# Performance work log

Hardware: AMD Instinct MI355X
Metric: run time of the kernel (lower is better)

The kernel has to match this reference:

```python
import jax, jax.numpy as jnp
import numpy as np

N, F_IN, HID, NH1, NCLS = 8192, 256, 64, 4, 16
LRELU_ALPHA = 0.2  # tf.nn.leaky_relu default


def setup_inputs() -> dict:
    key = jax.random.key(0)
    ks = jax.random.split(key, 12)
    s = 0.05
    seq = jax.random.normal(ks[0], (1, N, F_IN), jnp.float32)
    # sparse-ish adjacency -> additive mask bias (0 on edges, -1e9 elsewhere)
    adj = jax.random.uniform(ks[1], (N, N)) < 0.005
    adj = adj | jnp.eye(N, dtype=bool)
    bias_mat = jnp.where(adj, 0.0, -1e9).astype(jnp.float32)[None]  # [1,N,N]
    return {
        "seq": seq,
        "bias_mat": bias_mat,
        "W1": jax.random.normal(ks[2], (NH1, F_IN, HID), jnp.float32) * s,
        "a1_src": jax.random.normal(ks[3], (NH1, HID, 1), jnp.float32) * s,
        "a1_dst": jax.random.normal(ks[4], (NH1, HID, 1), jnp.float32) * s,
        "b1_src": jnp.zeros((NH1, 1), jnp.float32),
        "b1_dst": jnp.zeros((NH1, 1), jnp.float32),
        "bias1": jnp.zeros((NH1, HID), jnp.float32),
        "W2": jax.random.normal(ks[5], (1, NH1 * HID, NCLS), jnp.float32) * s,
        "a2_src": jax.random.normal(ks[6], (1, NCLS, 1), jnp.float32) * s,
        "a2_dst": jax.random.normal(ks[7], (1, NCLS, 1), jnp.float32) * s,
        "b2_src": jnp.zeros((1, 1), jnp.float32),
        "b2_dst": jnp.zeros((1, 1), jnp.float32),
        "bias2": jnp.zeros((1, NCLS), jnp.float32),
    }


def _gat_layer(x, bias_mat, W, a_src, a_dst, b_src, b_dst, bias_out):
    # x: [N, Fin]; W: [nh, Fin, H]; bias_mat: [1, N, N]
    fts = jnp.einsum('nf,hfd->hnd', x, W)                      # Conv1D(k=1, no bias)
    f1 = jnp.einsum('hnd,hdo->hno', fts, a_src) + b_src[:, None, :]  # [nh,N,1]
    f2 = jnp.einsum('hnd,hdo->hno', fts, a_dst) + b_dst[:, None, :]  # [nh,N,1]
    logits = f1 + jnp.swapaxes(f2, 1, 2)                       # [nh,N,N]
    coefs = jax.nn.softmax(jax.nn.leaky_relu(logits, LRELU_ALPHA) + bias_mat, axis=-1)
    vals = jnp.einsum('hnm,hmd->hnd', coefs, fts)              # [nh,N,H]
    return vals + bias_out[:, None, :]


def reference(seq, bias_mat, W1, a1_src, a1_dst, b1_src, b1_dst, bias1,
              W2, a2_src, a2_dst, b2_src, b2_dst, bias2):
    x = seq[0]  # [N, F_IN]; batch dim is 1
    # layer 1: NH1 heads, elu activation, concat over heads
    h = jax.nn.elu(_gat_layer(x, bias_mat, W1, a1_src, a1_dst, b1_src, b1_dst, bias1))
    h1 = jnp.transpose(h, (1, 0, 2)).reshape(N, NH1 * HID)     # tf.concat(heads, -1)
    # output layer: 1 head, identity activation, averaged over final heads (=1)
    out = _gat_layer(h1, bias_mat, W2, a2_src, a2_dst, b2_src, b2_dst, bias2)
    logits = out[0] / 1.0                                      # add_n/final_sum
    return logits[None]  # [1, N, NCLS]
```

## Files before the change

### kernel.cpp

```cpp
#include <hip/hip_runtime.h>
#include <hip/hip_bf16.h>
#include <math.h>

#define NN   8192
#define FIN  256
#define HID  64
#define NH   4
#define NC   16
#define MAXD 128
#define ALPHA 0.2f

__global__ __launch_bounds__(256) void k_scan_gemm(
    const float* __restrict__ bias, const float* __restrict__ seq,
    const float* __restrict__ W1, const float* __restrict__ a1s,
    const float* __restrict__ a1d, const float* __restrict__ b1s,
    const float* __restrict__ b1d,
    int* __restrict__ deg, int* __restrict__ cols,
    float* __restrict__ fts1, float* __restrict__ f1v, float* __restrict__ f2v)
{
    __shared__ float xs[64][68];
    __shared__ union {
        float w[64][68];
        struct { float r1[64][17]; float r2[64][17]; } red;
    } U;

    const int bid = blockIdx.x;
    const int t   = threadIdx.x;

    if (bid >= 512) {
        const int wv = t >> 6, lane = t & 63;
        const int row = (bid - 512) * 4 + wv;
        const float4* rp = (const float4*)(bias + (size_t)row * NN);
        int* crow = cols + (size_t)row * MAXD;
        const unsigned long long lt = (1ull << lane) - 1ull;
        int base = 0;
        for (int mit = 0; mit < 8; ++mit) {
            float4 vv[4];
            #pragma unroll
            for (int q = 0; q < 4; ++q) vv[q] = rp[mit*256 + q*64 + lane];
            #pragma unroll
            for (int q = 0; q < 4; ++q) {
                const float4 v = vv[q];
                const unsigned long long m0 = __ballot(v.x == 0.f);
                const unsigned long long m1 = __ballot(v.y == 0.f);
                const unsigned long long m2 = __ballot(v.z == 0.f);
                const unsigned long long m3 = __ballot(v.w == 0.f);
                int p = base + __popcll(m0&lt) + __popcll(m1&lt)
                             + __popcll(m2&lt) + __popcll(m3&lt);
                const int colbase = mit*1024 + q*256 + lane*4;
                if (v.x == 0.f) { if (p < MAXD) crow[p] = colbase;     ++p; }
                if (v.y == 0.f) { if (p < MAXD) crow[p] = colbase + 1; ++p; }
                if (v.z == 0.f) { if (p < MAXD) crow[p] = colbase + 2; ++p; }
                if (v.w == 0.f) { if (p < MAXD) crow[p] = colbase + 3; ++p; }
                base += __popcll(m0) + __popcll(m1) + __popcll(m2) + __popcll(m3);
            }
        }
        if (lane == 0) deg[row] = base < MAXD ? base : MAXD;
        return;
    }

    const int head    = bid & 3;
    const int rowbase = (bid >> 2) * 64;
    const int tr = t >> 4, tc = t & 15;

    float acc[4][4] = {};
    for (int kc = 0; kc < 4; ++kc) {
        #pragma unroll
        for (int i = 0; i < 4; ++i) {
            const int lin = t + i*256;
            const int r = lin >> 4, kq = lin & 15;
            const float4 v = *(const float4*)(seq + (size_t)(rowbase + r)*FIN + kc*64 + kq*4);
            *(float4*)&xs[r][kq*4] = v;
        }
        #pragma unroll
        for (int i = 0; i < 4; ++i) {
            const int lin = t + i*256;
            const int k = lin >> 4, dq = lin & 15;
            const float4 v = *(const float4*)(W1 + ((size_t)head*FIN + kc*64 + k)*HID + dq*4);
            *(float4*)&U.w[k][dq*4] = v;
        }
        __syncthreads();
        #pragma unroll 8
        for (int k = 0; k < 64; ++k) {
            const float4 bb = *(const float4*)&U.w[k][tc*4];
            #pragma unroll
            for (int i = 0; i < 4; ++i) {
                const float a = xs[tr*4 + i][k];
                acc[i][0] += a * bb.x; acc[i][1] += a * bb.y;
                acc[i][2] += a * bb.z; acc[i][3] += a * bb.w;
            }
        }
        __syncthreads();
    }

    float p1[4], p2[4];
    #pragma unroll
    for (int i = 0; i < 4; ++i) {
        const int node = rowbase + tr*4 + i;
        float4 o; o.x = acc[i][0]; o.y = acc[i][1]; o.z = acc[i][2]; o.w = acc[i][3];
        *(float4*)&fts1[((size_t)node*NH + head)*HID + tc*4] = o;
        float s1 = 0.f, s2 = 0.f;
        #pragma unroll
        for (int j = 0; j < 4; ++j) {
            s1 += acc[i][j] * a1s[head*HID + tc*4 + j];
            s2 += acc[i][j] * a1d[head*HID + tc*4 + j];
        }
        p1[i] = s1; p2[i] = s2;
    }
    #pragma unroll
    for (int i = 0; i < 4; ++i) {
        U.red.r1[tr*4 + i][tc] = p1[i];
        U.red.r2[tr*4 + i][tc] = p2[i];
    }
    __syncthreads();
    if (t < 64) {
        float s1 = b1s[head], s2 = b1d[head];
        #pragma unroll
        for (int q = 0; q < 16; ++q) { s1 += U.red.r1[t][q]; s2 += U.red.r2[t][q]; }
        const int node = rowbase + t;
        f1v[node*NH + head] = s1;
        f2v[node*NH + head] = s2;
    }
}

__global__ __launch_bounds__(256) void k_attn1(
    const float* __restrict__ fts1, const float* __restrict__ f1v,
    const float* __restrict__ f2v, const float* __restrict__ bias1,
    const float* __restrict__ W2, const float* __restrict__ a2s,
    const float* __restrict__ a2d, const float* __restrict__ b2s,
    const float* __restrict__ b2d,
    const int* __restrict__ deg, const int* __restrict__ cols,
    float* __restrict__ fts2, float* __restrict__ g1, float* __restrict__ g2)
{
    __shared__ int   colsS[MAXD];
    __shared__ float coefS[NH][MAXD];
    __shared__ float h1row[NH*HID];
    __shared__ float red[16][17];
    __shared__ float fts2S[NC];

    const int i = blockIdx.x;
    const int t = threadIdx.x, h = t >> 6, lane = t & 63;
    const int d = deg[i];
    for (int e = t; e < MAXD; e += 256) colsS[e] = (e < d) ? cols[(size_t)i*MAXD + e] : 0;
    __syncthreads();

    const float f1i = f1v[i*NH + h];
    float sc0 = -1e30f, sc1 = -1e30f;
    if (lane < d)      { const float x = f1i + f2v[colsS[lane]*NH + h];    sc0 = x > 0.f ? x : ALPHA*x; }
    if (lane + 64 < d) { const float x = f1i + f2v[colsS[lane+64]*NH + h]; sc1 = x > 0.f ? x : ALPHA*x; }
    float m = fmaxf(sc0, sc1);
    #pragma unroll
    for (int off = 32; off; off >>= 1) m = fmaxf(m, __shfl_xor(m, off));
    const float p0 = (lane      < d) ? expf(sc0 - m) : 0.f;
    const float p1 = (lane + 64 < d) ? expf(sc1 - m) : 0.f;
    coefS[h][lane] = p0; coefS[h][lane + 64] = p1;
    float sum = p0 + p1;
    #pragma unroll
    for (int off = 32; off; off >>= 1) sum += __shfl_xor(sum, off);
    const float inv = 1.f / sum;

    float acc = 0.f;
    #pragma unroll 4
    for (int e = 0; e < d; ++e)
        acc += coefS[h][e] * fts1[((size_t)colsS[e]*NH + h)*HID + lane];

    const float v = acc*inv + bias1[h*HID + lane];
    h1row[h*HID + lane] = v > 0.f ? v : expm1f(v);
    __syncthreads();

    {
        const int c = t & 15, part = t >> 4;
        float s = 0.f;
        #pragma unroll
        for (int q = 0; q < 16; ++q) s += h1row[part*16 + q] * W2[(part*16 + q)*NC + c];
        red[part][c] = s;
    }
    __syncthreads();
    if (t < NC) {
        float s = 0.f;
        #pragma unroll
        for (int q = 0; q < 16; ++q) s += red[q][t];
        fts2S[t] = s;
        fts2[(size_t)i*NC + t] = s;
    }
    __syncthreads();
    if (t == 0) {
        float s1 = b2s[0], s2 = b2d[0];
        #pragma unroll
        for (int c = 0; c < NC; ++c) { s1 += fts2S[c]*a2s[c]; s2 += fts2S[c]*a2d[c]; }
        g1[i] = s1; g2[i] = s2;
    }
}

__global__ __launch_bounds__(256) void k_attn2(
    const float* __restrict__ fts2, const float* __restrict__ g1,
    const float* __restrict__ g2, const float* __restrict__ bias2,
    const int* __restrict__ deg, const int* __restrict__ cols,
    float* __restrict__ out)
{
    __shared__ int   colsS[4][MAXD];
    __shared__ float coefS[4][MAXD];
    const int t = threadIdx.x, w = t >> 6, lane = t & 63;
    const int i = blockIdx.x*4 + w;
    const int d = deg[i];
    for (int e = lane; e < MAXD; e += 64) colsS[w][e] = (e < d) ? cols[(size_t)i*MAXD + e] : 0;

    const float g1i = g1[i];
    float sc0 = -1e30f, sc1 = -1e30f;
    if (lane < d)      { const float x = g1i + g2[colsS[w][lane]];    sc0 = x > 0.f ? x : ALPHA*x; }
    if (lane + 64 < d) { const float x = g1i + g2[colsS[w][lane+64]]; sc1 = x > 0.f ? x : ALPHA*x; }
    float m = fmaxf(sc0, sc1);
    #pragma unroll
    for (int off = 32; off; off >>= 1) m = fmaxf(m, __shfl_xor(m, off));
    const float p0 = (lane      < d) ? expf(sc0 - m) : 0.f;
    const float p1 = (lane + 64 < d) ? expf(sc1 - m) : 0.f;
    coefS[w][lane] = p0; coefS[w][lane + 64] = p1;
    float sum = p0 + p1;
    #pragma unroll
    for (int off = 32; off; off >>= 1) sum += __shfl_xor(sum, off);
    const float inv = 1.f / sum;

    if (lane < NC) {
        float acc = 0.f;
        #pragma unroll 4
        for (int e = 0; e < d; ++e)
            acc += coefS[w][e] * fts2[(size_t)colsS[w][e]*NC + lane];
        out[(size_t)i*NC + lane] = acc*inv + bias2[lane];
    }
}

extern "C" void kernel_launch(void* const* d_in, const int* in_sizes, int n_in,
                              void* d_out, int out_size, void* d_ws, size_t ws_size,
                              hipStream_t stream)
{
    const float* seq   = (const float*)d_in[0];
    const float* bias  = (const float*)d_in[1];
    const float* W1    = (const float*)d_in[2];
    const float* a1s   = (const float*)d_in[3];
    const float* a1d   = (const float*)d_in[4];
    const float* b1s   = (const float*)d_in[5];
    const float* b1d   = (const float*)d_in[6];
    const float* bias1 = (const float*)d_in[7];
    const float* W2    = (const float*)d_in[8];
    const float* a2s   = (const float*)d_in[9];
    const float* a2d   = (const float*)d_in[10];
    const float* b2s   = (const float*)d_in[11];
    const float* b2d   = (const float*)d_in[12];
    const float* bias2 = (const float*)d_in[13];

    char* ws = (char*)d_ws;
    int*   deg  = (int*)ws;    ws += (size_t)NN * 4;
    int*   cols = (int*)ws;    ws += (size_t)NN * MAXD * 4;
    float* fts1 = (float*)ws;  ws += (size_t)NN * NH * HID * 4;
    float* f1v  = (float*)ws;  ws += (size_t)NN * NH * 4;
    float* f2v  = (float*)ws;  ws += (size_t)NN * NH * 4;
    float* fts2 = (float*)ws;  ws += (size_t)NN * NC * 4;
    float* g1   = (float*)ws;  ws += (size_t)NN * 4;
    float* g2   = (float*)ws;  ws += (size_t)NN * 4;

    hipLaunchKernelGGL(k_scan_gemm, dim3(512 + 2048), dim3(256), 0, stream,
                       bias, seq, W1, a1s, a1d, b1s, b1d, deg, cols, fts1, f1v, f2v);
    hipLaunchKernelGGL(k_attn1, dim3(NN), dim3(256), 0, stream,
                       fts1, f1v, f2v, bias1, W2, a2s, a2d, b2s, b2d, deg, cols,
                       fts2, g1, g2);
    hipLaunchKernelGGL(k_attn2, dim3(NN/4), dim3(256), 0, stream,
                       fts2, g1, g2, bias2, deg, cols, (float*)d_out);
}
```

Measured before the change: 109.8 us.

## Fuse adjacency-bias scan into layer-1 attention kernel and parallelize layer-2 aggregation

The bias-row scan that builds neighbor lists moves out of the GEMM kernel and into the layer-1 attention kernel. Each block now scans its own row with a shared-memory atomic counter and uses the column list straight from LDS, so the attention no longer waits on a global cols round trip. The layer-2 aggregation spreads edges across all 64 lanes in groups of 4 and reduces with shuffles, instead of using only 16 lanes. Neighbor order becomes nondeterministic because of the atomics, which can slightly change the floating-point summation order.

```diff
diff --git a/kernel.cpp b/kernel.cpp
--- a/kernel.cpp
+++ b/kernel.cpp
@@ -10,12 +10,10 @@
 #define MAXD 128
 #define ALPHA 0.2f
 
-__global__ __launch_bounds__(256) void k_scan_gemm(
-    const float* __restrict__ bias, const float* __restrict__ seq,
-    const float* __restrict__ W1, const float* __restrict__ a1s,
-    const float* __restrict__ a1d, const float* __restrict__ b1s,
-    const float* __restrict__ b1d,
-    int* __restrict__ deg, int* __restrict__ cols,
+__global__ __launch_bounds__(256) void k_gemm(
+    const float* __restrict__ seq, const float* __restrict__ W1,
+    const float* __restrict__ a1s, const float* __restrict__ a1d,
+    const float* __restrict__ b1s, const float* __restrict__ b1d,
     float* __restrict__ fts1, float* __restrict__ f1v, float* __restrict__ f2v)
 {
     __shared__ float xs[64][68];
@@ -26,39 +24,6 @@
 
     const int bid = blockIdx.x;
     const int t   = threadIdx.x;
-
-    if (bid >= 512) {
-        const int wv = t >> 6, lane = t & 63;
-        const int row = (bid - 512) * 4 + wv;
-        const float4* rp = (const float4*)(bias + (size_t)row * NN);
-        int* crow = cols + (size_t)row * MAXD;
-        const unsigned long long lt = (1ull << lane) - 1ull;
-        int base = 0;
-        for (int mit = 0; mit < 8; ++mit) {
-            float4 vv[4];
-            #pragma unroll
-            for (int q = 0; q < 4; ++q) vv[q] = rp[mit*256 + q*64 + lane];
-            #pragma unroll
-            for (int q = 0; q < 4; ++q) {
-                const float4 v = vv[q];
-                const unsigned long long m0 = __ballot(v.x == 0.f);
-                const unsigned long long m1 = __ballot(v.y == 0.f);
-                const unsigned long long m2 = __ballot(v.z == 0.f);
-                const unsigned long long m3 = __ballot(v.w == 0.f);
-                int p = base + __popcll(m0&lt) + __popcll(m1&lt)
-                             + __popcll(m2&lt) + __popcll(m3&lt);
-                const int colbase = mit*1024 + q*256 + lane*4;
-                if (v.x == 0.f) { if (p < MAXD) crow[p] = colbase;     ++p; }
-                if (v.y == 0.f) { if (p < MAXD) crow[p] = colbase + 1; ++p; }
-                if (v.z == 0.f) { if (p < MAXD) crow[p] = colbase + 2; ++p; }
-                if (v.w == 0.f) { if (p < MAXD) crow[p] = colbase + 3; ++p; }
-                base += __popcll(m0) + __popcll(m1) + __popcll(m2) + __popcll(m3);
-            }
-        }
-        if (lane == 0) deg[row] = base < MAXD ? base : MAXD;
-        return;
-    }
-
     const int head    = bid & 3;
     const int rowbase = (bid >> 2) * 64;
     const int tr = t >> 4, tc = t & 15;
@@ -123,16 +88,17 @@
     }
 }
 
-__global__ __launch_bounds__(256) void k_attn1(
-    const float* __restrict__ fts1, const float* __restrict__ f1v,
-    const float* __restrict__ f2v, const float* __restrict__ bias1,
-    const float* __restrict__ W2, const float* __restrict__ a2s,
-    const float* __restrict__ a2d, const float* __restrict__ b2s,
-    const float* __restrict__ b2d,
-    const int* __restrict__ deg, const int* __restrict__ cols,
+__global__ __launch_bounds__(256) void k_scan_attn1(
+    const float* __restrict__ bias, const float* __restrict__ fts1,
+    const float* __restrict__ f1v, const float* __restrict__ f2v,
+    const float* __restrict__ bias1, const float* __restrict__ W2,
+    const float* __restrict__ a2s, const float* __restrict__ a2d,
+    const float* __restrict__ b2s, const float* __restrict__ b2d,
+    int* __restrict__ deg, int* __restrict__ cols,
     float* __restrict__ fts2, float* __restrict__ g1, float* __restrict__ g2)
 {
     __shared__ int   colsS[MAXD];
+    __shared__ int   cnt;
     __shared__ float coefS[NH][MAXD];
     __shared__ float h1row[NH*HID];
     __shared__ float red[16][17];
@@ -140,9 +106,27 @@
 
     const int i = blockIdx.x;
     const int t = threadIdx.x, h = t >> 6, lane = t & 63;
-    const int d = deg[i];
-    for (int e = t; e < MAXD; e += 256) colsS[e] = (e < d) ? cols[(size_t)i*MAXD + e] : 0;
-    __syncthreads();
+    if (t == 0) cnt = 0;
+    if (t < MAXD) colsS[t] = 0;
+    __syncthreads();
+
+    const float4* rp = (const float4*)(bias + (size_t)i * NN);
+    float4 vv[8];
+    #pragma unroll
+    for (int k = 0; k < 8; ++k) vv[k] = rp[k*256 + t];
+    #pragma unroll
+    for (int k = 0; k < 8; ++k) {
+        const float4 v = vv[k];
+        const int cb = (k*256 + t) * 4;
+        if (v.x == 0.f) { int p = atomicAdd(&cnt, 1); if (p < MAXD) colsS[p] = cb;     }
+        if (v.y == 0.f) { int p = atomicAdd(&cnt, 1); if (p < MAXD) colsS[p] = cb + 1; }
+        if (v.z == 0.f) { int p = atomicAdd(&cnt, 1); if (p < MAXD) colsS[p] = cb + 2; }
+        if (v.w == 0.f) { int p = atomicAdd(&cnt, 1); if (p < MAXD) colsS[p] = cb + 3; }
+    }
+    __syncthreads();
+    const int d = cnt < MAXD ? cnt : MAXD;
+    if (t < MAXD) cols[(size_t)i*MAXD + t] = colsS[t];
+    if (t == 0)   deg[i] = d;
 
     const float f1i = f1v[i*NH + h];
     float sc0 = -1e30f, sc1 = -1e30f;
@@ -160,7 +144,7 @@
     const float inv = 1.f / sum;
 
     float acc = 0.f;
-    #pragma unroll 4
+    #pragma unroll 8
     for (int e = 0; e < d; ++e)
         acc += coefS[h][e] * fts1[((size_t)colsS[e]*NH + h)*HID + lane];
 
@@ -220,13 +204,16 @@
     for (int off = 32; off; off >>= 1) sum += __shfl_xor(sum, off);
     const float inv = 1.f / sum;
 
-    if (lane < NC) {
-        float acc = 0.f;
-        #pragma unroll 4
-        for (int e = 0; e < d; ++e)
-            acc += coefS[w][e] * fts2[(size_t)colsS[w][e]*NC + lane];
-        out[(size_t)i*NC + lane] = acc*inv + bias2[lane];
-    }
+    const int eg = lane >> 4, c = lane & 15;
+    float acc = 0.f;
+    #pragma unroll 2
+    for (int e0 = 0; e0 < d; e0 += 4) {
+        const int e = e0 + eg;
+        if (e < d) acc += coefS[w][e] * fts2[(size_t)colsS[w][e]*NC + c];
+    }
+    acc += __shfl_xor(acc, 16);
+    acc += __shfl_xor(acc, 32);
+    if (lane < NC) out[(size_t)i*NC + lane] = acc*inv + bias2[lane];
 }
 
 extern "C" void kernel_launch(void* const* d_in, const int* in_sizes, int n_in,
@@ -258,11 +245,11 @@
     float* g1   = (float*)ws;  ws += (size_t)NN * 4;
     float* g2   = (float*)ws;  ws += (size_t)NN * 4;
 
-    hipLaunchKernelGGL(k_scan_gemm, dim3(512 + 2048), dim3(256), 0, stream,
-                       bias, seq, W1, a1s, a1d, b1s, b1d, deg, cols, fts1, f1v, f2v);
-    hipLaunchKernelGGL(k_attn1, dim3(NN), dim3(256), 0, stream,
-                       fts1, f1v, f2v, bias1, W2, a2s, a2d, b2s, b2d, deg, cols,
-                       fts2, g1, g2);
+    hipLaunchKernelGGL(k_gemm, dim3(512), dim3(256), 0, stream,
+                       seq, W1, a1s, a1d, b1s, b1d, fts1, f1v, f2v);
+    hipLaunchKernelGGL(k_scan_attn1, dim3(NN), dim3(256), 0, stream,
+                       bias, fts1, f1v, f2v, bias1, W2, a2s, a2d, b2s, b2d,
+                       deg, cols, fts2, g1, g2);
     hipLaunchKernelGGL(k_attn2, dim3(NN/4), dim3(256), 0, stream,
                        fts2, g1, g2, bias2, deg, cols, (float*)d_out);
 }
```

Measured after the change: 115.4 us. 5.1% more time.
